# Kernel tuning notes

Hardware: AMD Instinct MI355X
Metric: run time of the kernel (lower is better)

## Reference

```python
import jax, jax.numpy as jnp
import numpy as np

N_NODES = 100000
N_EDGES = 1600000
D = 32  # atom and bond feature dim


def _mlp(x, W1, b1, W2, b2, W3, b3):
    # fff: Linear(in,128) -> ReLU -> Linear(128,64) -> ReLU -> Linear(64,32)
    h = jax.nn.relu(x @ W1 + b1)
    h = jax.nn.relu(h @ W2 + b2)
    return h @ W3 + b3


def _init_mlp(key, in_dim):
    ks = jax.random.split(key, 3)
    def lin(k, fan_in, fan_out):
        bound = 1.0 / np.sqrt(fan_in)
        kw, kb = jax.random.split(k)
        W = jax.random.uniform(kw, (fan_in, fan_out), jnp.float32, -bound, bound)
        b = jax.random.uniform(kb, (fan_out,), jnp.float32, -bound, bound)
        return W, b
    W1, b1 = lin(ks[0], in_dim, 128)
    W2, b2 = lin(ks[1], 128, 64)
    W3, b3 = lin(ks[2], 64, 32)
    return W1, b1, W2, b2, W3, b3


def setup_inputs() -> dict:
    key = jax.random.key(0)
    k_bonds, k_a1, k_a2, k_atoms, k_e, k_v = jax.random.split(key, 6)
    inp = {
        "bonds": jax.random.normal(k_bonds, (N_EDGES, D), jnp.float32),
        "bond_atom_1": jax.random.randint(k_a1, (N_EDGES,), 0, N_NODES, jnp.int64),
        "bond_atom_2": jax.random.randint(k_a2, (N_EDGES,), 0, N_NODES, jnp.int64),
        "atoms": jax.random.normal(k_atoms, (N_NODES, D), jnp.float32),
    }
    We1, be1, We2, be2, We3, be3 = _init_mlp(k_e, 96)
    Wv1, bv1, Wv2, bv2, Wv3, bv3 = _init_mlp(k_v, 64)
    inp.update(We1=We1, be1=be1, We2=We2, be2=be2, We3=We3, be3=be3,
               Wv1=Wv1, bv1=bv1, Wv2=Wv2, bv2=bv2, Wv3=Wv3, bv3=bv3)
    return inp


def reference(bonds, bond_atom_1, bond_atom_2, atoms,
              We1, be1, We2, be2, We3, be3,
              Wv1, bv1, Wv2, bv2, Wv3, bv3):
    # Edge update: gather endpoint atom features, concat with bond feats, MLP
    atom1 = atoms[bond_atom_1]                    # [E, D]
    atom2 = atoms[bond_atom_2]                    # [E, D]
    e_in = jnp.concatenate([atom1, atom2, bonds], axis=1)  # [E, 3D]
    new_bonds = _mlp(e_in, We1, be1, We2, be2, We3, be3)    # [E, 32]

    # Node update: scatter-mean new bond features onto target atoms
    # (PyG default flow aggregates messages at edge_index[1] == bond_atom_2)
    n = atoms.shape[0]
    seg_sum = jax.ops.segment_sum(new_bonds, bond_atom_2, num_segments=n)
    counts = jax.ops.segment_sum(jnp.ones((new_bonds.shape[0],), new_bonds.dtype),
                                 bond_atom_2, num_segments=n)
    mean_bonds = seg_sum / jnp.maximum(counts, 1.0)[:, None]  # [N, 32]

    v_in = jnp.concatenate([mean_bonds, atoms], axis=1)        # [N, 64]
    new_atoms = _mlp(v_in, Wv1, bv1, Wv2, bv2, Wv3, bv3)       # [N, 32]
    return (new_atoms, new_bonds)
```

## Files before the change

kernel.cpp:

```cpp
#include <hip/hip_runtime.h>
#include <hip/hip_bf16.h>

#define NN 100000
#define NE 1600000
#define NB_SCAN 391
#define ETILES 12500
#define EGRID 512
#define NGRID 1024

typedef __attribute__((ext_vector_type(8))) short bfrag8;
typedef __attribute__((ext_vector_type(4))) float f32x4;
typedef __attribute__((ext_vector_type(8))) unsigned short us8;
typedef __attribute__((ext_vector_type(4))) unsigned int u32x4;

__device__ __forceinline__ unsigned short f2bf(float f) {
  unsigned int u = __float_as_uint(f);
  u += 0x7fffu + ((u >> 16) & 1u);
  return (unsigned short)(u >> 16);
}

__device__ __forceinline__ unsigned int pk2(float a, float b) {
  unsigned int r;
  asm("v_cvt_pk_bf16_f32 %0, %1, %2" : "=v"(r) : "v"(a), "v"(b));
  return r;
}

__device__ __forceinline__ uint2 pk4(float v0, float v1, float v2, float v3) {
  return make_uint2(pk2(v0, v1), pk2(v2, v3));
}

__device__ __forceinline__ bfrag8 pack8(float4 a, float4 b) {
  union { u32x4 u; bfrag8 f; } c;
  c.u[0] = pk2(a.x, a.y); c.u[1] = pk2(a.z, a.w);
  c.u[2] = pk2(b.x, b.y); c.u[3] = pk2(b.z, b.w);
  return c.f;
}

__device__ __forceinline__ bfrag8 as_frag(us8 v) {
  union { us8 u; bfrag8 f; } c;
  c.u = v;
  return c.f;
}

__device__ __forceinline__ float bl(unsigned int u) { return __uint_as_float(u << 16); }
__device__ __forceinline__ float bh(unsigned int u) { return __uint_as_float(u & 0xffff0000u); }

__device__ __forceinline__ f32x4 mfma16(bfrag8 a, bfrag8 b, f32x4 c) {
  return __builtin_amdgcn_mfma_f32_16x16x32_bf16(a, b, c, 0, 0, 0);
}

__device__ __forceinline__ void gload_lds16(const void* g, void* l) {
  __builtin_amdgcn_global_load_lds(
      (const __attribute__((address_space(1))) unsigned int*)g,
      (__attribute__((address_space(3))) unsigned int*)l, 16, 0, 0);
}

__global__ void prep(const float* __restrict__ atoms, unsigned short* __restrict__ atoms_bf,
                     const int* __restrict__ a2, int* __restrict__ cnt,
                     const float* __restrict__ We1, const float* __restrict__ We2,
                     const float* __restrict__ We3, const float* __restrict__ Wv1,
                     const float* __restrict__ Wv2, const float* __restrict__ Wv3,
                     unsigned short* __restrict__ wp) {
  const int b = blockIdx.x, tid = threadIdx.x;
  if (b < 3125) {
    const int i = b * 256 + tid;
    float4 v = *(const float4*)(atoms + (size_t)i * 4);
    *(uint2*)(atoms_bf + (size_t)i * 4) = pk4(v.x, v.y, v.z, v.w);
  } else if (b < 3125 + 6250) {
    const int e = (b - 3125) * 256 + tid;
    if (e < NE) atomicAdd(&cnt[a2[e]], 1);
  } else {
    const int i = (b - 9375) * 256 + tid;
    const float* src; int base, N;
    if (i < 12288)      { src = We1; base = 0;     N = 128; }
    else if (i < 20480) { src = We2; base = 12288; N = 64;  }
    else if (i < 22528) { src = We3; base = 20480; N = 32;  }
    else if (i < 30720) { src = Wv1; base = 22528; N = 128; }
    else if (i < 38912) { src = Wv2; base = 30720; N = 64;  }
    else                { src = Wv3; base = 38912; N = 32;  }
    const int il = i - base;
    const int j = il & 7, gc = il >> 3;
    const int c = gc % N, g = gc / N;
    wp[i] = f2bf(src[(g * 8 + j) * N + c]);
  }
}

__global__ void scan_blocks(const int* __restrict__ cnt, int* __restrict__ off,
                            int* __restrict__ bsum) {
  __shared__ int s[256];
  const int t = threadIdx.x;
  const int idx = blockIdx.x * 256 + t;
  int v = (idx < NN) ? cnt[idx] : 0;
  s[t] = v;
  __syncthreads();
  for (int d = 1; d < 256; d <<= 1) {
    int x = (t >= d) ? s[t - d] : 0;
    __syncthreads();
    s[t] += x;
    __syncthreads();
  }
  if (idx < NN) off[idx] = s[t] - v;
  if (t == 255) bsum[blockIdx.x] = s[255];
}

__global__ void scan_finalize(int* __restrict__ off, const int* __restrict__ bsum,
                              int* __restrict__ cursor) {
  __shared__ int red[256];
  const int b = blockIdx.x, t = threadIdx.x;
  int s = 0;
  for (int k = t; k < b; k += 256) s += bsum[k];
  red[t] = s;
  __syncthreads();
  for (int d = 128; d > 0; d >>= 1) {
    if (t < d) red[t] += red[t + d];
    __syncthreads();
  }
  const int base = red[0];
  const int idx = b * 256 + t;
  if (idx < NN) {
    int o = off[idx] + base;
    off[idx] = o;
    cursor[idx] = o;
  }
  if (idx == 0) off[NN] = NE;
}

__global__ void fill_k(const int* __restrict__ a2, int* __restrict__ cursor,
                       int* __restrict__ buf, int mode) {
  int e = blockIdx.x * 256 + threadIdx.x;
  if (e < NE) {
    int p = atomicAdd(&cursor[a2[e]], 1);
    if (mode) buf[e] = p;
    else buf[p] = e;
  }
}

template <int FAST>
__global__ __launch_bounds__(256, 2) void edge_kernel(
    const float* __restrict__ bonds, const int* __restrict__ a1p, const int* __restrict__ a2p,
    const unsigned short* __restrict__ atoms_bf,
    const float* __restrict__ be1, const float* __restrict__ be2, const float* __restrict__ be3,
    const unsigned short* __restrict__ wpack,
    float* __restrict__ new_bonds,
    const int* __restrict__ pos, unsigned short* __restrict__ nb_bf) {
  __shared__ unsigned short sW[22528];
  __shared__ float sB1[128], sB2[64], sB3[32];
  __shared__ unsigned short sH1[128 * 136];

  const int tid = threadIdx.x;
  const int lane = tid & 63, wv = tid >> 6;
  const int cl = lane & 15, q = lane >> 4;
  const int esub = wv * 32 + cl;

  {
    const char* src = (const char*)wpack;
    char* dst = (char*)sW;
#pragma unroll
    for (int i = 0; i < 11; ++i) {
      const int c = i * 4 + wv;
      gload_lds16(src + c * 1024 + lane * 16, dst + c * 1024);
    }
  }
  if (tid < 128) sB1[tid] = be1[tid];
  else if (tid < 192) sB2[tid - 128] = be2[tid - 128];
  else if (tid < 224) sB3[tid - 192] = be3[tid - 192];

  int tile = blockIdx.x;
  us8 ra1[2], ra2[2];
  float4 rb[2][2];
  int ia1n[2], ia2n[2];
  int slotc = 0;

#pragma unroll
  for (int t = 0; t < 2; ++t) {
    const int e = tile * 128 + esub + t * 16;
    const int ia1 = a1p[e], ia2 = a2p[e];
    ra1[t] = *(const us8*)(atoms_bf + (size_t)ia1 * 32 + q * 8);
    ra2[t] = *(const us8*)(atoms_bf + (size_t)ia2 * 32 + q * 8);
    const float* bp = bonds + (size_t)e * 32 + q * 8;
    rb[t][0] = *(const float4*)(bp);
    rb[t][1] = *(const float4*)(bp + 4);
  }
  if (FAST && tid < 128) slotc = pos[tile * 128 + tid];
  {
    int tn = tile + EGRID; if (tn >= ETILES) tn = tile;
#pragma unroll
    for (int t = 0; t < 2; ++t) {
      const int e = tn * 128 + esub + t * 16;
      ia1n[t] = a1p[e]; ia2n[t] = a2p[e];
    }
  }
  __syncthreads();

  for (; tile < ETILES; tile += EGRID) {
    bfrag8 xb0[2], xb1[2], xb2[2];
#pragma unroll
    for (int t = 0; t < 2; ++t) {
      xb0[t] = as_frag(ra1[t]);
      xb1[t] = as_frag(ra2[t]);
      xb2[t] = pack8(rb[t][0], rb[t][1]);
    }
    const int tn = (tile + EGRID < ETILES) ? tile + EGRID : tile;
#pragma unroll
    for (int t = 0; t < 2; ++t) {
      ra1[t] = *(const us8*)(atoms_bf + (size_t)ia1n[t] * 32 + q * 8);
      ra2[t] = *(const us8*)(atoms_bf + (size_t)ia2n[t] * 32 + q * 8);
      const int e = tn * 128 + esub + t * 16;
      const float* bp = bonds + (size_t)e * 32 + q * 8;
      rb[t][0] = *(const float4*)(bp);
      rb[t][1] = *(const float4*)(bp + 4);
    }
    int slotn = 0;
    if (FAST && tid < 128) slotn = pos[tn * 128 + tid];
    {
      int tnn = tile + 2 * EGRID; if (tnn >= ETILES) tnn = tn;
#pragma unroll
      for (int t = 0; t < 2; ++t) {
        const int e = tnn * 128 + esub + t * 16;
        ia1n[t] = a1p[e]; ia2n[t] = a2p[e];
      }
    }

#pragma unroll
    for (int rt = 0; rt < 8; ++rt) {
      const unsigned short* wa = &sW[(q * 128 + rt * 16 + cl) * 8];
      bfrag8 w0 = *(const bfrag8*)(wa);
      bfrag8 w1 = *(const bfrag8*)(wa + 4096);
      bfrag8 w2 = *(const bfrag8*)(wa + 8192);
      f32x4 acc[2];
      acc[0] = (f32x4){0.f, 0.f, 0.f, 0.f};
      acc[1] = (f32x4){0.f, 0.f, 0.f, 0.f};
#pragma unroll
      for (int t = 0; t < 2; ++t) {
        acc[t] = mfma16(w0, xb0[t], acc[t]);
        acc[t] = mfma16(w1, xb1[t], acc[t]);
        acc[t] = mfma16(w2, xb2[t], acc[t]);
      }
      const int c0 = rt * 16 + q * 4;
#pragma unroll
      for (int t = 0; t < 2; ++t) {
        uint2 hv = pk4(fmaxf(acc[t][0] + sB1[c0 + 0], 0.f),
                       fmaxf(acc[t][1] + sB1[c0 + 1], 0.f),
                       fmaxf(acc[t][2] + sB1[c0 + 2], 0.f),
                       fmaxf(acc[t][3] + sB1[c0 + 3], 0.f));
        *(uint2*)&sH1[(esub + t * 16) * 136 + c0] = hv;
      }
    }
    __syncthreads();

    bfrag8 hb[4][2];
#pragma unroll
    for (int t = 0; t < 2; ++t) {
      const unsigned short* hr = &sH1[(esub + t * 16) * 136 + q * 8];
#pragma unroll
      for (int ks = 0; ks < 4; ++ks) hb[ks][t] = *(const bfrag8*)(hr + ks * 32);
    }
    __syncthreads();

    unsigned short* sH2 = sH1;
#pragma unroll
    for (int rt = 0; rt < 4; ++rt) {
      f32x4 acc[2];
      acc[0] = (f32x4){0.f, 0.f, 0.f, 0.f};
      acc[1] = (f32x4){0.f, 0.f, 0.f, 0.f};
#pragma unroll
      for (int ks = 0; ks < 4; ++ks) {
        bfrag8 w = *(const bfrag8*)&sW[12288 + ks * 2048 + (q * 64 + rt * 16 + cl) * 8];
#pragma unroll
        for (int t = 0; t < 2; ++t) acc[t] = mfma16(w, hb[ks][t], acc[t]);
      }
      const int c0 = rt * 16 + q * 4;
#pragma unroll
      for (int t = 0; t < 2; ++t) {
        uint2 hv = pk4(fmaxf(acc[t][0] + sB2[c0 + 0], 0.f),
                       fmaxf(acc[t][1] + sB2[c0 + 1], 0.f),
                       fmaxf(acc[t][2] + sB2[c0 + 2], 0.f),
                       fmaxf(acc[t][3] + sB2[c0 + 3], 0.f));
        *(uint2*)&sH2[(esub + t * 16) * 72 + c0] = hv;
      }
    }
    __syncthreads();

    bfrag8 gb0[2], gb1[2];
#pragma unroll
    for (int t = 0; t < 2; ++t) {
      const unsigned short* hr = &sH2[(esub + t * 16) * 72 + q * 8];
      gb0[t] = *(const bfrag8*)(hr);
      gb1[t] = *(const bfrag8*)(hr + 32);
    }
    unsigned short* sOut = sH1 + 9216;
#pragma unroll
    for (int rt = 0; rt < 2; ++rt) {
      bfrag8 w0 = *(const bfrag8*)&sW[20480 + (q * 32 + rt * 16 + cl) * 8];
      bfrag8 w1 = *(const bfrag8*)&sW[20480 + 1024 + (q * 32 + rt * 16 + cl) * 8];
      const int c0 = rt * 16 + q * 4;
#pragma unroll
      for (int t = 0; t < 2; ++t) {
        f32x4 acc = {0.f, 0.f, 0.f, 0.f};
        acc = mfma16(w0, gb0[t], acc);
        acc = mfma16(w1, gb1[t], acc);
        const int e = tile * 128 + esub + t * 16;
        float4 o;
        o.x = acc[0] + sB3[c0 + 0];
        o.y = acc[1] + sB3[c0 + 1];
        o.z = acc[2] + sB3[c0 + 2];
        o.w = acc[3] + sB3[c0 + 3];
        *(float4*)(new_bonds + (size_t)e * 32 + c0) = o;
        if (FAST) {
          *(uint2*)&sOut[(esub + t * 16) * 40 + c0] =
              make_uint2(pk2(o.x, o.y), pk2(o.z, o.w));
        }
      }
    }
    if (FAST) {
      __syncthreads();
      if (tid < 128) {
        const u32x4* src = (const u32x4*)&sOut[tid * 40];
        u32x4* dst = (u32x4*)(nb_bf + (size_t)slotc * 32);
#pragma unroll
        for (int k = 0; k < 4; ++k) dst[k] = src[k];
      }
      slotc = slotn;
    }
    __syncthreads();
  }
}

__global__ __launch_bounds__(256, 8) void gather_seq(
    const int* __restrict__ off, const unsigned short* __restrict__ nb_bf,
    unsigned short* __restrict__ mean_bf) {
  const int gt = blockIdx.x * 256 + threadIdx.x;
  const int n = gt >> 3, sl = gt & 7;
  const int o0 = off[n], o1 = off[n + 1];
  const int deg = o1 - o0;
  float s0 = 0.f, s1 = 0.f, s2 = 0.f, s3 = 0.f;
  const unsigned short* p = nb_bf + (size_t)o0 * 32 + sl * 4;
  int i = 0;
  for (; i + 1 < deg; i += 2) {
    uint2 a = *(const uint2*)(p);
    uint2 b = *(const uint2*)(p + 32);
    p += 64;
    s0 += bl(a.x) + bl(b.x); s1 += bh(a.x) + bh(b.x);
    s2 += bl(a.y) + bl(b.y); s3 += bh(a.y) + bh(b.y);
  }
  if (i < deg) {
    uint2 a = *(const uint2*)(p);
    s0 += bl(a.x); s1 += bh(a.x); s2 += bl(a.y); s3 += bh(a.y);
  }
  const float inv = 1.0f / fmaxf((float)deg, 1.0f);
  *(uint2*)(mean_bf + (size_t)n * 32 + sl * 4) =
      make_uint2(pk2(s0 * inv, s1 * inv), pk2(s2 * inv, s3 * inv));
}

__global__ __launch_bounds__(256, 8) void gather_rand(
    const int* __restrict__ off, const int* __restrict__ csr,
    const float* __restrict__ new_bonds, float* __restrict__ mean_f32) {
  const int tid = blockIdx.x * 256 + threadIdx.x;
  const int n = tid >> 3, sl = tid & 7;
  const int o0 = off[n], o1 = off[n + 1];
  float4 s0 = {0.f, 0.f, 0.f, 0.f}, s1 = {0.f, 0.f, 0.f, 0.f};
  int i = o0;
  for (; i + 1 < o1; i += 2) {
    const int ea = csr[i], eb = csr[i + 1];
    float4 a = *(const float4*)(new_bonds + (size_t)ea * 32 + sl * 4);
    float4 b = *(const float4*)(new_bonds + (size_t)eb * 32 + sl * 4);
    s0.x += a.x; s0.y += a.y; s0.z += a.z; s0.w += a.w;
    s1.x += b.x; s1.y += b.y; s1.z += b.z; s1.w += b.w;
  }
  if (i < o1) {
    const int ea = csr[i];
    float4 a = *(const float4*)(new_bonds + (size_t)ea * 32 + sl * 4);
    s0.x += a.x; s0.y += a.y; s0.z += a.z; s0.w += a.w;
  }
  const float inv = 1.0f / fmaxf((float)(o1 - o0), 1.0f);
  float4 m;
  m.x = (s0.x + s1.x) * inv;
  m.y = (s0.y + s1.y) * inv;
  m.z = (s0.z + s1.z) * inv;
  m.w = (s0.w + s1.w) * inv;
  *(float4*)(mean_f32 + (size_t)n * 32 + sl * 4) = m;
}

template <int MODE>
__global__ __launch_bounds__(256, 4) void node_mlp(
    const unsigned short* __restrict__ atoms_bf,
    const float* __restrict__ bv1, const float* __restrict__ bv2, const float* __restrict__ bv3,
    const unsigned short* __restrict__ wpack,
    const void* __restrict__ mean_src, float* __restrict__ new_atoms) {
  __shared__ unsigned short sW[18432];
  __shared__ float sB1[128], sB2[64], sB3[32];
  __shared__ unsigned short sV[64 * 72];
  __shared__ unsigned short sH1[64 * 136];

  const int tid = threadIdx.x;
  const int lane = tid & 63, wv = tid >> 6;
  const int cl = lane & 15, q = lane >> 4;
  const int nl = tid >> 2, l4 = tid & 3;

  {
    const uint4* src = (const uint4*)wpack;
    uint4* dst = (uint4*)sW;
#pragma unroll
    for (int i = 0; i < 9; ++i) dst[tid + i * 256] = src[tid + i * 256];
  }
  if (tid < 128) sB1[tid] = bv1[tid];
  if (tid < 64) sB2[tid] = bv2[tid];
  if (tid < 32) sB3[tid] = bv3[tid];

  for (int n0 = blockIdx.x * 64; n0 < NN; n0 += NGRID * 64) {
    __syncthreads();

    {
      const int n = n0 + nl;
      if (n < NN) {
        if (l4 < 2) {
          if (MODE == 1) {
            const unsigned short* mp = (const unsigned short*)mean_src + (size_t)n * 32 + l4 * 16;
            *(us8*)&sV[nl * 72 + l4 * 16] = *(const us8*)(mp);
            *(us8*)&sV[nl * 72 + l4 * 16 + 8] = *(const us8*)(mp + 8);
          } else {
            const float* sp = (const float*)mean_src + (size_t)n * 32 + l4 * 16;
            float4 a = *(const float4*)(sp);
            float4 b = *(const float4*)(sp + 4);
            float4 c = *(const float4*)(sp + 8);
            float4 d = *(const float4*)(sp + 12);
            uint4 o0, o1;
            o0.x = pk2(a.x, a.y); o0.y = pk2(a.z, a.w);
            o0.z = pk2(b.x, b.y); o0.w = pk2(b.z, b.w);
            o1.x = pk2(c.x, c.y); o1.y = pk2(c.z, c.w);
            o1.z = pk2(d.x, d.y); o1.w = pk2(d.z, d.w);
            *(uint4*)&sV[nl * 72 + l4 * 16] = o0;
            *(uint4*)&sV[nl * 72 + l4 * 16 + 8] = o1;
          }
        } else {
          const unsigned short* ap = atoms_bf + (size_t)n * 32 + (l4 - 2) * 16;
          *(us8*)&sV[nl * 72 + 32 + (l4 - 2) * 16] = *(const us8*)(ap);
          *(us8*)&sV[nl * 72 + 32 + (l4 - 2) * 16 + 8] = *(const us8*)(ap + 8);
        }
      } else {
        us8 z = {0, 0, 0, 0, 0, 0, 0, 0};
        *(us8*)&sV[nl * 72 + l4 * 16] = z;
        *(us8*)&sV[nl * 72 + l4 * 16 + 8] = z;
      }
    }
    __syncthreads();

    const int nt = wv * 16;
    const int ng = n0 + nt + cl;

    bfrag8 vb0 = *(const bfrag8*)&sV[(nt + cl) * 72 + q * 8];
    bfrag8 vb1 = *(const bfrag8*)&sV[(nt + cl) * 72 + 32 + q * 8];
#pragma unroll
    for (int rt = 0; rt < 8; ++rt) {
      f32x4 acc = {0.f, 0.f, 0.f, 0.f};
      acc = mfma16(*(const bfrag8*)&sW[(q * 128 + rt * 16 + cl) * 8], vb0, acc);
      acc = mfma16(*(const bfrag8*)&sW[4096 + (q * 128 + rt * 16 + cl) * 8], vb1, acc);
      const int c0 = rt * 16 + q * 4;
      uint2 hv = pk4(fmaxf(acc[0] + sB1[c0 + 0], 0.f),
                     fmaxf(acc[1] + sB1[c0 + 1], 0.f),
                     fmaxf(acc[2] + sB1[c0 + 2], 0.f),
                     fmaxf(acc[3] + sB1[c0 + 3], 0.f));
      *(uint2*)&sH1[(nt + cl) * 136 + c0] = hv;
    }
    __syncthreads();

    bfrag8 hb[4];
    {
      const unsigned short* hr = &sH1[(nt + cl) * 136 + q * 8];
#pragma unroll
      for (int ks = 0; ks < 4; ++ks) hb[ks] = *(const bfrag8*)(hr + ks * 32);
    }
    __syncthreads();
#pragma unroll
    for (int rt = 0; rt < 4; ++rt) {
      f32x4 acc = {0.f, 0.f, 0.f, 0.f};
#pragma unroll
      for (int ks = 0; ks < 4; ++ks)
        acc = mfma16(*(const bfrag8*)&sW[8192 + ks * 2048 + (q * 64 + rt * 16 + cl) * 8], hb[ks], acc);
      const int c0 = rt * 16 + q * 4;
      uint2 hv = pk4(fmaxf(acc[0] + sB2[c0 + 0], 0.f),
                     fmaxf(acc[1] + sB2[c0 + 1], 0.f),
                     fmaxf(acc[2] + sB2[c0 + 2], 0.f),
                     fmaxf(acc[3] + sB2[c0 + 3], 0.f));
      *(uint2*)&sV[(nt + cl) * 72 + c0] = hv;
    }
    __syncthreads();

    bfrag8 gb0 = *(const bfrag8*)&sV[(nt + cl) * 72 + q * 8];
    bfrag8 gb1 = *(const bfrag8*)&sV[(nt + cl) * 72 + 32 + q * 8];
    if (ng < NN) {
      float* outp = new_atoms + (size_t)ng * 32;
#pragma unroll
      for (int rt = 0; rt < 2; ++rt) {
        f32x4 acc = {0.f, 0.f, 0.f, 0.f};
        acc = mfma16(*(const bfrag8*)&sW[16384 + (q * 32 + rt * 16 + cl) * 8], gb0, acc);
        acc = mfma16(*(const bfrag8*)&sW[16384 + 1024 + (q * 32 + rt * 16 + cl) * 8], gb1, acc);
        const int c0 = rt * 16 + q * 4;
        float4 o;
        o.x = acc[0] + sB3[c0 + 0];
        o.y = acc[1] + sB3[c0 + 1];
        o.z = acc[2] + sB3[c0 + 2];
        o.w = acc[3] + sB3[c0 + 3];
        *(float4*)(outp + c0) = o;
      }
    }
  }
}

extern "C" void kernel_launch(void* const* d_in, const int* in_sizes, int n_in,
                              void* d_out, int out_size, void* d_ws, size_t ws_size,
                              hipStream_t stream) {
  const float* bonds = (const float*)d_in[0];
  const int* a1 = (const int*)d_in[1];
  const int* a2 = (const int*)d_in[2];
  const float* atoms = (const float*)d_in[3];
  const float* We1 = (const float*)d_in[4];
  const float* be1 = (const float*)d_in[5];
  const float* We2 = (const float*)d_in[6];
  const float* be2 = (const float*)d_in[7];
  const float* We3 = (const float*)d_in[8];
  const float* be3 = (const float*)d_in[9];
  const float* Wv1 = (const float*)d_in[10];
  const float* bv1 = (const float*)d_in[11];
  const float* Wv2 = (const float*)d_in[12];
  const float* bv2 = (const float*)d_in[13];
  const float* Wv3 = (const float*)d_in[14];
  const float* bv3 = (const float*)d_in[15];

  float* out = (float*)d_out;
  float* new_atoms = out;
  float* new_bonds = out + (size_t)NN * 32;

  char* ws = (char*)d_ws;
  int* cnt    = (int*)(ws + 0);
  int* off    = (int*)(ws + 400000);
  int* bsum   = (int*)(ws + 800016);
  unsigned short* wp = (unsigned short*)(ws + 802064);
  int* poscsr = (int*)(ws + 883984);
  unsigned short* atoms_bf = (unsigned short*)(ws + 7283984);
  unsigned short* mean_bf  = (unsigned short*)(ws + 13683984);
  unsigned short* nb_bf    = (unsigned short*)(ws + 20083984);

  const int fast = (ws_size >= (size_t)122483984) ? 1 : 0;

  hipMemsetAsync(cnt, 0, (size_t)NN * 4, stream);

  prep<<<9535, 256, 0, stream>>>(atoms, atoms_bf, a2, cnt,
                                 We1, We2, We3, Wv1, Wv2, Wv3, wp);

  scan_blocks<<<NB_SCAN, 256, 0, stream>>>(cnt, off, bsum);
  scan_finalize<<<NB_SCAN, 256, 0, stream>>>(off, bsum, cnt);
  fill_k<<<(NE + 255) / 256, 256, 0, stream>>>(a2, cnt, poscsr, fast);

  if (fast) {
    edge_kernel<1><<<EGRID, 256, 0, stream>>>(bonds, a1, a2, atoms_bf, be1, be2, be3, wp,
                                              new_bonds, poscsr, nb_bf);
    gather_seq<<<NN * 8 / 256, 256, 0, stream>>>(off, nb_bf, mean_bf);
    node_mlp<1><<<NGRID, 256, 0, stream>>>(atoms_bf, bv1, bv2, bv3, wp + 22528,
                                           mean_bf, new_atoms);
  } else {
    edge_kernel<0><<<EGRID, 256, 0, stream>>>(bonds, a1, a2, atoms_bf, be1, be2, be3, wp,
                                              new_bonds, nullptr, nullptr);
    gather_rand<<<NN * 8 / 256, 256, 0, stream>>>(off, poscsr, new_bonds, new_atoms);
    node_mlp<0><<<NGRID, 256, 0, stream>>>(atoms_bf, bv1, bv2, bv3, wp + 22528,
                                           new_atoms, new_atoms);
  }
}
```

Baseline: 382.8 us.

## Pass MLP activations between layers via wave shuffles instead of LDS

The edge kernel no longer stages hidden activations in a large shared-memory buffer. It rebuilds the MFMA B-operand fragments for each layer with cross-lane shuffles of the packed bf16 outputs. This drops the per-tile __syncthreads barriers and cuts LDS use, which allows raising occupancy to 3 blocks per CU, and the persistent grid grows to match. The sorted bf16 copy is now written straight from registers by every lane, with its slot loaded per tile. In exchange there are many more ds_bpermute/shuffle ops and higher register pressure under the tighter launch bound.

Result: slower. 442.5 us (+15.6%).

```diff
diff --git a/kernel.cpp b/kernel.cpp
--- a/kernel.cpp
+++ b/kernel.cpp
@@ -5,7 +5,7 @@
 #define NE 1600000
 #define NB_SCAN 391
 #define ETILES 12500
-#define EGRID 512
+#define EGRID 768
 #define NGRID 1024
 
 typedef __attribute__((ext_vector_type(8))) short bfrag8;
@@ -40,6 +40,16 @@
   union { us8 u; bfrag8 f; } c;
   c.u = v;
   return c.f;
+}
+
+__device__ __forceinline__ bfrag8 as_frag_u(u32x4 v) {
+  union { u32x4 u; bfrag8 f; } c;
+  c.u = v;
+  return c.f;
+}
+
+__device__ __forceinline__ unsigned int sh(unsigned int v, int src) {
+  return (unsigned int)__shfl((int)v, src, 64);
 }
 
 __device__ __forceinline__ float bl(unsigned int u) { return __uint_as_float(u << 16); }
@@ -136,7 +146,7 @@
 }
 
 template <int FAST>
-__global__ __launch_bounds__(256, 2) void edge_kernel(
+__global__ __launch_bounds__(256, 3) void edge_kernel(
     const float* __restrict__ bonds, const int* __restrict__ a1p, const int* __restrict__ a2p,
     const unsigned short* __restrict__ atoms_bf,
     const float* __restrict__ be1, const float* __restrict__ be2, const float* __restrict__ be3,
@@ -145,12 +155,14 @@
     const int* __restrict__ pos, unsigned short* __restrict__ nb_bf) {
   __shared__ unsigned short sW[22528];
   __shared__ float sB1[128], sB2[64], sB3[32];
-  __shared__ unsigned short sH1[128 * 136];
 
   const int tid = threadIdx.x;
   const int lane = tid & 63, wv = tid >> 6;
   const int cl = lane & 15, q = lane >> 4;
   const int esub = wv * 32 + cl;
+  const int srcA = cl + ((q & 1) << 5);
+  const int srcB = srcA + 16;
+  const bool hi = (lane & 32) != 0;
 
   {
     const char* src = (const char*)wpack;
@@ -169,7 +181,6 @@
   us8 ra1[2], ra2[2];
   float4 rb[2][2];
   int ia1n[2], ia2n[2];
-  int slotc = 0;
 
 #pragma unroll
   for (int t = 0; t < 2; ++t) {
@@ -181,7 +192,6 @@
     rb[t][0] = *(const float4*)(bp);
     rb[t][1] = *(const float4*)(bp + 4);
   }
-  if (FAST && tid < 128) slotc = pos[tile * 128 + tid];
   {
     int tn = tile + EGRID; if (tn >= ETILES) tn = tile;
 #pragma unroll
@@ -210,8 +220,6 @@
       rb[t][0] = *(const float4*)(bp);
       rb[t][1] = *(const float4*)(bp + 4);
     }
-    int slotn = 0;
-    if (FAST && tid < 128) slotn = pos[tn * 128 + tid];
     {
       int tnn = tile + 2 * EGRID; if (tnn >= ETILES) tnn = tn;
 #pragma unroll
@@ -221,108 +229,123 @@
       }
     }
 
+    unsigned int hp[2][8][2];
 #pragma unroll
     for (int rt = 0; rt < 8; ++rt) {
       const unsigned short* wa = &sW[(q * 128 + rt * 16 + cl) * 8];
       bfrag8 w0 = *(const bfrag8*)(wa);
       bfrag8 w1 = *(const bfrag8*)(wa + 4096);
       bfrag8 w2 = *(const bfrag8*)(wa + 8192);
-      f32x4 acc[2];
-      acc[0] = (f32x4){0.f, 0.f, 0.f, 0.f};
-      acc[1] = (f32x4){0.f, 0.f, 0.f, 0.f};
-#pragma unroll
-      for (int t = 0; t < 2; ++t) {
-        acc[t] = mfma16(w0, xb0[t], acc[t]);
-        acc[t] = mfma16(w1, xb1[t], acc[t]);
-        acc[t] = mfma16(w2, xb2[t], acc[t]);
-      }
       const int c0 = rt * 16 + q * 4;
 #pragma unroll
       for (int t = 0; t < 2; ++t) {
-        uint2 hv = pk4(fmaxf(acc[t][0] + sB1[c0 + 0], 0.f),
-                       fmaxf(acc[t][1] + sB1[c0 + 1], 0.f),
-                       fmaxf(acc[t][2] + sB1[c0 + 2], 0.f),
-                       fmaxf(acc[t][3] + sB1[c0 + 3], 0.f));
-        *(uint2*)&sH1[(esub + t * 16) * 136 + c0] = hv;
-      }
-    }
-    __syncthreads();
-
-    bfrag8 hb[4][2];
-#pragma unroll
-    for (int t = 0; t < 2; ++t) {
-      const unsigned short* hr = &sH1[(esub + t * 16) * 136 + q * 8];
-#pragma unroll
-      for (int ks = 0; ks < 4; ++ks) hb[ks][t] = *(const bfrag8*)(hr + ks * 32);
-    }
-    __syncthreads();
-
-    unsigned short* sH2 = sH1;
+        f32x4 acc = {0.f, 0.f, 0.f, 0.f};
+        acc = mfma16(w0, xb0[t], acc);
+        acc = mfma16(w1, xb1[t], acc);
+        acc = mfma16(w2, xb2[t], acc);
+        hp[t][rt][0] = pk2(fmaxf(acc[0] + sB1[c0 + 0], 0.f),
+                           fmaxf(acc[1] + sB1[c0 + 1], 0.f));
+        hp[t][rt][1] = pk2(fmaxf(acc[2] + sB1[c0 + 2], 0.f),
+                           fmaxf(acc[3] + sB1[c0 + 3], 0.f));
+      }
+    }
+
+    f32x4 acc2[2][4];
+#pragma unroll
+    for (int t = 0; t < 2; ++t)
+#pragma unroll
+      for (int rt = 0; rt < 4; ++rt) acc2[t][rt] = (f32x4){0.f, 0.f, 0.f, 0.f};
+#pragma unroll
+    for (int ks = 0; ks < 4; ++ks) {
+      bfrag8 hb[2];
+#pragma unroll
+      for (int t = 0; t < 2; ++t) {
+        u32x4 bw;
+        unsigned int x, y;
+        x = sh(hp[t][2 * ks][0], srcA); y = sh(hp[t][2 * ks + 1][0], srcA); bw[0] = hi ? y : x;
+        x = sh(hp[t][2 * ks][1], srcA); y = sh(hp[t][2 * ks + 1][1], srcA); bw[1] = hi ? y : x;
+        x = sh(hp[t][2 * ks][0], srcB); y = sh(hp[t][2 * ks + 1][0], srcB); bw[2] = hi ? y : x;
+        x = sh(hp[t][2 * ks][1], srcB); y = sh(hp[t][2 * ks + 1][1], srcB); bw[3] = hi ? y : x;
+        hb[t] = as_frag_u(bw);
+      }
+#pragma unroll
+      for (int rt = 0; rt < 4; ++rt) {
+        bfrag8 w = *(const bfrag8*)&sW[12288 + ks * 2048 + (q * 64 + rt * 16 + cl) * 8];
+#pragma unroll
+        for (int t = 0; t < 2; ++t) acc2[t][rt] = mfma16(w, hb[t], acc2[t][rt]);
+      }
+    }
+    unsigned int hp2[2][4][2];
 #pragma unroll
     for (int rt = 0; rt < 4; ++rt) {
-      f32x4 acc[2];
-      acc[0] = (f32x4){0.f, 0.f, 0.f, 0.f};
-      acc[1] = (f32x4){0.f, 0.f, 0.f, 0.f};
-#pragma unroll
-      for (int ks = 0; ks < 4; ++ks) {
-        bfrag8 w = *(const bfrag8*)&sW[12288 + ks * 2048 + (q * 64 + rt * 16 + cl) * 8];
-#pragma unroll
-        for (int t = 0; t < 2; ++t) acc[t] = mfma16(w, hb[ks][t], acc[t]);
-      }
       const int c0 = rt * 16 + q * 4;
 #pragma unroll
       for (int t = 0; t < 2; ++t) {
-        uint2 hv = pk4(fmaxf(acc[t][0] + sB2[c0 + 0], 0.f),
-                       fmaxf(acc[t][1] + sB2[c0 + 1], 0.f),
-                       fmaxf(acc[t][2] + sB2[c0 + 2], 0.f),
-                       fmaxf(acc[t][3] + sB2[c0 + 3], 0.f));
-        *(uint2*)&sH2[(esub + t * 16) * 72 + c0] = hv;
-      }
-    }
-    __syncthreads();
-
-    bfrag8 gb0[2], gb1[2];
-#pragma unroll
-    for (int t = 0; t < 2; ++t) {
-      const unsigned short* hr = &sH2[(esub + t * 16) * 72 + q * 8];
-      gb0[t] = *(const bfrag8*)(hr);
-      gb1[t] = *(const bfrag8*)(hr + 32);
-    }
-    unsigned short* sOut = sH1 + 9216;
+        hp2[t][rt][0] = pk2(fmaxf(acc2[t][rt][0] + sB2[c0 + 0], 0.f),
+                            fmaxf(acc2[t][rt][1] + sB2[c0 + 1], 0.f));
+        hp2[t][rt][1] = pk2(fmaxf(acc2[t][rt][2] + sB2[c0 + 2], 0.f),
+                            fmaxf(acc2[t][rt][3] + sB2[c0 + 3], 0.f));
+      }
+    }
+
+    f32x4 acc3[2][2];
+#pragma unroll
+    for (int t = 0; t < 2; ++t)
+#pragma unroll
+      for (int rt = 0; rt < 2; ++rt) acc3[t][rt] = (f32x4){0.f, 0.f, 0.f, 0.f};
+#pragma unroll
+    for (int ks = 0; ks < 2; ++ks) {
+      bfrag8 gb[2];
+#pragma unroll
+      for (int t = 0; t < 2; ++t) {
+        u32x4 bw;
+        unsigned int x, y;
+        x = sh(hp2[t][2 * ks][0], srcA); y = sh(hp2[t][2 * ks + 1][0], srcA); bw[0] = hi ? y : x;
+        x = sh(hp2[t][2 * ks][1], srcA); y = sh(hp2[t][2 * ks + 1][1], srcA); bw[1] = hi ? y : x;
+        x = sh(hp2[t][2 * ks][0], srcB); y = sh(hp2[t][2 * ks + 1][0], srcB); bw[2] = hi ? y : x;
+        x = sh(hp2[t][2 * ks][1], srcB); y = sh(hp2[t][2 * ks + 1][1], srcB); bw[3] = hi ? y : x;
+        gb[t] = as_frag_u(bw);
+      }
+#pragma unroll
+      for (int rt = 0; rt < 2; ++rt) {
+        bfrag8 w = *(const bfrag8*)&sW[20480 + ks * 1024 + (q * 32 + rt * 16 + cl) * 8];
+#pragma unroll
+        for (int t = 0; t < 2; ++t) acc3[t][rt] = mfma16(w, gb[t], acc3[t][rt]);
+      }
+    }
+
+    unsigned int hp3[2][2][2];
 #pragma unroll
     for (int rt = 0; rt < 2; ++rt) {
-      bfrag8 w0 = *(const bfrag8*)&sW[20480 + (q * 32 + rt * 16 + cl) * 8];
-      bfrag8 w1 = *(const bfrag8*)&sW[20480 + 1024 + (q * 32 + rt * 16 + cl) * 8];
       const int c0 = rt * 16 + q * 4;
 #pragma unroll
       for (int t = 0; t < 2; ++t) {
-        f32x4 acc = {0.f, 0.f, 0.f, 0.f};
-        acc = mfma16(w0, gb0[t], acc);
-        acc = mfma16(w1, gb1[t], acc);
+        float4 o;
+        o.x = acc3[t][rt][0] + sB3[c0 + 0];
+        o.y = acc3[t][rt][1] + sB3[c0 + 1];
+        o.z = acc3[t][rt][2] + sB3[c0 + 2];
+        o.w = acc3[t][rt][3] + sB3[c0 + 3];
         const int e = tile * 128 + esub + t * 16;
-        float4 o;
-        o.x = acc[0] + sB3[c0 + 0];
-        o.y = acc[1] + sB3[c0 + 1];
-        o.z = acc[2] + sB3[c0 + 2];
-        o.w = acc[3] + sB3[c0 + 3];
         *(float4*)(new_bonds + (size_t)e * 32 + c0) = o;
         if (FAST) {
-          *(uint2*)&sOut[(esub + t * 16) * 40 + c0] =
-              make_uint2(pk2(o.x, o.y), pk2(o.z, o.w));
+          hp3[t][rt][0] = pk2(o.x, o.y);
+          hp3[t][rt][1] = pk2(o.z, o.w);
         }
       }
     }
     if (FAST) {
-      __syncthreads();
-      if (tid < 128) {
-        const u32x4* src = (const u32x4*)&sOut[tid * 40];
-        u32x4* dst = (u32x4*)(nb_bf + (size_t)slotc * 32);
-#pragma unroll
-        for (int k = 0; k < 4; ++k) dst[k] = src[k];
-      }
-      slotc = slotn;
-    }
-    __syncthreads();
+#pragma unroll
+      for (int t = 0; t < 2; ++t) {
+        const int slot = pos[tile * 128 + wv * 32 + t * 16 + cl];
+        u32x4 W;
+        unsigned int x, y;
+        x = sh(hp3[t][0][0], srcA); y = sh(hp3[t][1][0], srcA); W[0] = hi ? y : x;
+        x = sh(hp3[t][0][1], srcA); y = sh(hp3[t][1][1], srcA); W[1] = hi ? y : x;
+        x = sh(hp3[t][0][0], srcB); y = sh(hp3[t][1][0], srcB); W[2] = hi ? y : x;
+        x = sh(hp3[t][0][1], srcB); y = sh(hp3[t][1][1], srcB); W[3] = hi ? y : x;
+        *(u32x4*)(nb_bf + (size_t)slot * 32 + q * 8) = W;
+      }
+    }
   }
 }
 
```
